# Performance work log

Measured on AMD Instinct MI355X. Metric: run time of the kernel, lower is better.

The kernel has to match this reference:

```python
import jax, jax.numpy as jnp
import numpy as np

N_CELLS = 50000
N_GENES = 2000
HIDDEN = 128
HEADS = 4
HEAD_DIM = HIDDEN // HEADS
E_FULL = 800000
E_PRUNED = 400000
LN_EPS = 1e-6
NEG_SLOPE = 0.2


def setup_inputs() -> dict:
    key = jax.random.key(0)
    ks = jax.random.split(key, 20)
    s_in = 1.0 / np.sqrt(N_GENES)
    s_h = 1.0 / np.sqrt(HIDDEN)
    inp = {
        "node_features": jax.random.normal(ks[0], (N_CELLS, N_GENES), jnp.float32),
        "full_edge_index": jax.random.randint(ks[1], (2, E_FULL), 0, N_CELLS, jnp.int64 if jax.config.jax_enable_x64 else jnp.int32),
        "full_edge_weights": jax.random.uniform(ks[2], (E_FULL, 1), jnp.float32),
        "pruned_edge_index": jax.random.randint(ks[3], (2, E_PRUNED), 0, N_CELLS, jnp.int64 if jax.config.jax_enable_x64 else jnp.int32),
        "pruned_edge_weights": jax.random.uniform(ks[4], (E_PRUNED, 1), jnp.float32),
        "alpha": jax.random.uniform(ks[5], (), jnp.float32),
        # input projection
        "ip_w": jax.random.normal(ks[6], (N_GENES, HIDDEN), jnp.float32) * s_in,
        "ip_b": jnp.zeros((HIDDEN,), jnp.float32),
        # GAT full graph
        "gf_wsrc": jax.random.normal(ks[7], (HIDDEN, HIDDEN), jnp.float32) * s_h,
        "gf_wdst": jax.random.normal(ks[8], (HIDDEN, HIDDEN), jnp.float32) * s_h,
        "gf_wedge": jax.random.normal(ks[9], (1, HIDDEN), jnp.float32),
        "gf_attn": jax.random.normal(ks[10], (HEADS, HEAD_DIM), jnp.float32) * (1.0 / np.sqrt(HEAD_DIM)),
        "gf_bias": jnp.zeros((HIDDEN,), jnp.float32),
        # GAT pruned graph
        "gp_wsrc": jax.random.normal(ks[11], (HIDDEN, HIDDEN), jnp.float32) * s_h,
        "gp_wdst": jax.random.normal(ks[12], (HIDDEN, HIDDEN), jnp.float32) * s_h,
        "gp_wedge": jax.random.normal(ks[13], (1, HIDDEN), jnp.float32),
        "gp_attn": jax.random.normal(ks[14], (HEADS, HEAD_DIM), jnp.float32) * (1.0 / np.sqrt(HEAD_DIM)),
        "gp_bias": jnp.zeros((HIDDEN,), jnp.float32),
        # LayerNorm
        "ln_scale": jnp.ones((HIDDEN,), jnp.float32),
        "ln_bias": jnp.zeros((HIDDEN,), jnp.float32),
    }
    return inp


def _gatv2(h, edge_index, edge_w, wsrc, wdst, wedge, attn, bias):
    """GATv2 with edge features: e_ij = a_h . leaky_relu(Ws h_i + Wd h_j + We w_ij),
    segment-softmax over destination nodes, scatter-aggregate Ws h_src, concat heads."""
    n = h.shape[0]
    src, dst = edge_index[0], edge_index[1]
    hs = (h @ wsrc).reshape(n, HEADS, HEAD_DIM)
    hd = (h @ wdst).reshape(n, HEADS, HEAD_DIM)
    ew = (edge_w @ wedge).reshape(-1, HEADS, HEAD_DIM)  # [E,H,D]
    z = jax.nn.leaky_relu(hs[src] + hd[dst] + ew, NEG_SLOPE)  # [E,H,D]
    logits = jnp.einsum('ehd,hd->eh', z, attn)  # [E,H]
    # segment softmax over incoming edges of each dst node
    m = jax.ops.segment_max(logits, dst, num_segments=n)
    m = jnp.where(jnp.isfinite(m), m, 0.0)
    ex = jnp.exp(logits - m[dst])
    denom = jax.ops.segment_sum(ex, dst, num_segments=n)
    att = ex / (denom[dst] + 1e-16)  # [E,H]
    out = jax.ops.segment_sum(att[..., None] * hs[src], dst, num_segments=n)  # [n,H,D]
    return out.reshape(n, HIDDEN) + bias


def _layer_norm(x, scale, bias):
    mu = jnp.mean(x, axis=-1, keepdims=True)
    var = jnp.mean(jnp.square(x - mu), axis=-1, keepdims=True)
    return (x - mu) * jax.lax.rsqrt(var + LN_EPS) * scale + bias


def reference(node_features, full_edge_index, full_edge_weights, pruned_edge_index,
              pruned_edge_weights, alpha, ip_w, ip_b,
              gf_wsrc, gf_wdst, gf_wedge, gf_attn, gf_bias,
              gp_wsrc, gp_wdst, gp_wedge, gp_attn, gp_bias,
              ln_scale, ln_bias):
    h = node_features @ ip_w + ip_b  # [n, hidden]
    h_full = _gatv2(h, full_edge_index, full_edge_weights, gf_wsrc, gf_wdst, gf_wedge, gf_attn, gf_bias)
    h_pruned = _gatv2(h, pruned_edge_index, pruned_edge_weights, gp_wsrc, gp_wdst, gp_wedge, gp_attn, gp_bias)
    h = (1.0 - alpha) * h_full + alpha * h_pruned
    h = jax.nn.elu(h)
    return _layer_norm(h, ln_scale, ln_bias)
```

## Files before the change

### kernel.cpp

```cpp
#include <hip/hip_runtime.h>

#define N_GENES 2000

typedef __attribute__((ext_vector_type(8))) short frag8;
typedef __attribute__((ext_vector_type(4))) float facc4;

static __device__ __forceinline__ unsigned short f2bf(float f) {
    unsigned int u = __float_as_uint(f);
    unsigned int r = (u + 0x7FFFu + ((u >> 16) & 1u)) >> 16;
    return (unsigned short)r;
}
static __device__ __forceinline__ float bf2f(unsigned short s) {
    return __uint_as_float(((unsigned int)s) << 16);
}

__global__ void transpose_bt(const float* __restrict__ W, unsigned short* __restrict__ Bt,
                             int K, int Kpad) {
    int idx = blockIdx.x * blockDim.x + threadIdx.x;
    if (idx >= 128 * Kpad) return;
    int nrow = idx / Kpad, k = idx - nrow * Kpad;
    unsigned short v = 0;
    if (k < K) v = f2bf(W[(size_t)k * 128 + nrow]);
    Bt[idx] = v;
}

__global__ void transpose_small(const float* __restrict__ ws_f, const float* __restrict__ wd_f,
                                const float* __restrict__ ws_p, const float* __restrict__ wd_p,
                                unsigned short* __restrict__ Bf, unsigned short* __restrict__ Bp) {
    int idx = blockIdx.x * blockDim.x + threadIdx.x;
    if (idx >= 2 * 256 * 128) return;
    int g = idx >> 15;
    int r = (idx >> 7) & 255;
    int k = idx & 127;
    const float* w = (g == 0) ? (r < 128 ? ws_f : wd_f) : (r < 128 ? ws_p : wd_p);
    unsigned short v = f2bf(w[k * 128 + (r & 127)]);
    (g == 0 ? Bf : Bp)[(r << 7) | k] = v;
}

#define SA 72

template <int AF32, int NT, int BIAS>
__global__ __launch_bounds__(256) void gemm64(const void* __restrict__ Av,
                                              const unsigned short* __restrict__ Bt,
                                              const float* __restrict__ bias,
                                              unsigned short* __restrict__ Cb,
                                              int M, int K, int Kpad) {
    __shared__ __align__(16) unsigned short lA[64 * SA];
    __shared__ __align__(16) unsigned short lB[NT * SA];
    constexpr int CF = NT / 64;
    int t = threadIdx.x, lane = t & 63, wv = t >> 6;
    int lr = lane & 15, lq = lane >> 4;
    facc4 acc[4][CF];
#pragma unroll
    for (int i = 0; i < 4; i++)
#pragma unroll
        for (int j = 0; j < CF; j++) acc[i][j] = (facc4){0.f, 0.f, 0.f, 0.f};
    int row_base = blockIdx.x * 64;

    for (int k0 = 0; k0 < Kpad; k0 += 64) {
        __syncthreads();
        if (AF32) {
            const float* A = (const float*)Av;
#pragma unroll
            for (int j = 0; j < 4; j++) {
                int q = j * 256 + t;
                int r = q >> 4, off = (q & 15) * 4;
                int rg = row_base + r; if (rg >= M) rg = M - 1;
                int kk = k0 + off;
                float4 v = {0.f, 0.f, 0.f, 0.f};
                if (kk < K) v = *(const float4*)(A + (size_t)rg * K + kk);
                ushort4 b;
                b.x = f2bf(v.x); b.y = f2bf(v.y); b.z = f2bf(v.z); b.w = f2bf(v.w);
                *(ushort4*)&lA[r * SA + off] = b;
            }
        } else {
            const unsigned short* A = (const unsigned short*)Av;
#pragma unroll
            for (int j = 0; j < 2; j++) {
                int q = j * 256 + t;
                int r = q >> 3, off = (q & 7) * 8;
                int rg = row_base + r; if (rg >= M) rg = M - 1;
                *(uint4*)&lA[r * SA + off] = *(const uint4*)(A + (size_t)rg * K + k0 + off);
            }
        }
#pragma unroll
        for (int j = 0; j < NT / 32; j++) {
            int q = j * 256 + t;
            int r = q >> 3, off = (q & 7) * 8;
            *(uint4*)&lB[r * SA + off] = *(const uint4*)(Bt + (size_t)r * Kpad + k0 + off);
        }
        __syncthreads();
#pragma unroll
        for (int ks = 0; ks < 2; ks++) {
            frag8 af[4], bf[CF];
#pragma unroll
            for (int mi = 0; mi < 4; mi++)
                af[mi] = *(const frag8*)&lA[(mi * 16 + lr) * SA + ks * 32 + lq * 8];
#pragma unroll
            for (int ni = 0; ni < CF; ni++)
                bf[ni] = *(const frag8*)&lB[(wv * 16 * CF + ni * 16 + lr) * SA + ks * 32 + lq * 8];
#pragma unroll
            for (int mi = 0; mi < 4; mi++)
#pragma unroll
                for (int ni = 0; ni < CF; ni++)
                    acc[mi][ni] = __builtin_amdgcn_mfma_f32_16x16x32_bf16(af[mi], bf[ni], acc[mi][ni], 0, 0, 0);
        }
    }
#pragma unroll
    for (int mi = 0; mi < 4; mi++) {
#pragma unroll
        for (int r = 0; r < 4; r++) {
            int row = row_base + mi * 16 + lq * 4 + r;
            if (row < M) {
#pragma unroll
                for (int ni = 0; ni < CF; ni++) {
                    int col = wv * 16 * CF + ni * 16 + lr;
                    float v = acc[mi][ni][r];
                    if (BIAS) v += bias[col];
                    Cb[(size_t)row * NT + col] = f2bf(v);
                }
            }
        }
    }
}

__global__ void deg2(const int* __restrict__ dst_f, int Ef,
                     const int* __restrict__ dst_p, int Ep,
                     int* __restrict__ deg, int N) {
    int e = blockIdx.x * blockDim.x + threadIdx.x;
    if (e < Ef) atomicAdd(&deg[dst_f[e]], 1);
    else if (e < Ef + Ep) atomicAdd(&deg[N + dst_p[e - Ef]], 1);
}

__global__ __launch_bounds__(256) void scan_part(const int* __restrict__ in,
                                                 int* __restrict__ bsum, int n) {
    int t = threadIdx.x, b = blockIdx.x;
    int lane = t & 63, wv = t >> 6;
    int base = b * 2048 + t * 8;
    int s = 0;
    if (base + 7 < n) {
        int4 v0 = *(const int4*)(in + base);
        int4 v1 = *(const int4*)(in + base + 4);
        s = v0.x + v0.y + v0.z + v0.w + v1.x + v1.y + v1.z + v1.w;
    } else {
#pragma unroll
        for (int j = 0; j < 8; j++) if (base + j < n) s += in[base + j];
    }
#pragma unroll
    for (int o = 32; o >= 1; o >>= 1) s += __shfl_xor(s, o);
    __shared__ int red[4];
    if (lane == 0) red[wv] = s;
    __syncthreads();
    if (t == 0) bsum[b] = red[0] + red[1] + red[2] + red[3];
}

__global__ __launch_bounds__(256) void scan_tops(int* __restrict__ bsum, int nb,
                                                 int* __restrict__ offs, int n) {
    __shared__ int buf[256];
    int t = threadIdx.x;
    int orig = (t < nb) ? bsum[t] : 0;
    int v = orig;
    buf[t] = v;
    __syncthreads();
    for (int o = 1; o < 256; o <<= 1) {
        int y = (t >= o) ? buf[t - o] : 0;
        __syncthreads();
        v += y;
        buf[t] = v;
        __syncthreads();
    }
    if (t < nb) bsum[t] = v - orig;
    if (t == nb - 1) offs[n] = v;
}

__global__ __launch_bounds__(256) void scan_final(const int* __restrict__ in,
                                                  const int* __restrict__ bsum,
                                                  int* __restrict__ offs, int n) {
    int t = threadIdx.x, b = blockIdx.x;
    int lane = t & 63, wv = t >> 6;
    int base = b * 2048 + t * 8;
    int a[8];
#pragma unroll
    for (int j = 0; j < 8; j++) a[j] = (base + j < n) ? in[base + j] : 0;
    int s = a[0] + a[1] + a[2] + a[3] + a[4] + a[5] + a[6] + a[7];
    int incl = s;
#pragma unroll
    for (int o = 1; o < 64; o <<= 1) {
        int y = __shfl_up(incl, o);
        if (lane >= o) incl += y;
    }
    __shared__ int wsum[4];
    if (lane == 63) wsum[wv] = incl;
    __syncthreads();
    int wpre = 0;
#pragma unroll
    for (int j = 0; j < 4; j++) if (j < wv) wpre += wsum[j];
    int excl = incl - s + wpre + bsum[b];
#pragma unroll
    for (int j = 0; j < 8; j++) {
        if (base + j < n) offs[base + j] = excl;
        excl += a[j];
    }
}

__global__ void fill2(const int* __restrict__ src_f, const int* __restrict__ dst_f,
                      const float* __restrict__ ew_f, int Ef,
                      const int* __restrict__ src_p, const int* __restrict__ dst_p,
                      const float* __restrict__ ew_p, int Ep,
                      const int* __restrict__ offs, int* __restrict__ cur,
                      int* __restrict__ srcs, float* __restrict__ ws, int N) {
    int e = blockIdx.x * blockDim.x + threadIdx.x;
    if (e >= Ef + Ep) return;
    int g = (e >= Ef);
    int ee = g ? e - Ef : e;
    int d = g ? dst_p[ee] : dst_f[ee];
    int node = g ? N + d : d;
    int p = offs[node] + atomicAdd(&cur[node], 1);
    srcs[p] = g ? src_p[ee] : src_f[ee];
    ws[p] = g ? ew_p[ee] : ew_f[ee];
}

__global__ __launch_bounds__(256) void gat_kernel(const int* __restrict__ offs,
                                                  const int* __restrict__ srcs,
                                                  const float* __restrict__ ws,
                                                  const unsigned short* __restrict__ hshd,
                                                  const float* __restrict__ wedge,
                                                  const float* __restrict__ attn,
                                                  const float* __restrict__ bias,
                                                  float* __restrict__ out, int n) {
    int node = blockIdx.x * 4 + (threadIdx.x >> 6);
    if (node >= n) return;
    int lane = threadIdx.x & 63;
    const float wv0 = wedge[lane], wv1 = wedge[lane + 64];
    const float a0 = attn[lane], a1 = attn[lane + 64];
    const unsigned short* hdrow = hshd + (size_t)node * 256 + 128;
    const float hd0 = bf2f(hdrow[lane]);
    const float hd1 = bf2f(hdrow[lane + 64]);
    int s = offs[node], cnt = offs[node + 1] - s;
    float m0 = -INFINITY, l0 = 0.f, acc0 = 0.f;
    float m1 = -INFINITY, l1 = 0.f, acc1 = 0.f;
    if (cnt > 0) {
        int last = s + cnt - 1;
        int jB = (s + 1 <= last) ? s + 1 : last;
        int srcA = srcs[s];       float wA = ws[s];
        int srcB = srcs[jB];      float wB = ws[jB];
        float hsA0 = bf2f(hshd[(size_t)srcA * 256 + lane]);
        float hsA1 = bf2f(hshd[(size_t)srcA * 256 + 64 + lane]);
        float hsB0 = bf2f(hshd[(size_t)srcB * 256 + lane]);
        float hsB1 = bf2f(hshd[(size_t)srcB * 256 + 64 + lane]);
        for (int i = 0; i < cnt; i++) {
            int jC = s + i + 2; if (jC > last) jC = last;
            int srcC = srcs[jC];  float wC = ws[jC];
            float hsC0 = bf2f(hshd[(size_t)srcC * 256 + lane]);
            float hsC1 = bf2f(hshd[(size_t)srcC * 256 + 64 + lane]);
            float z0 = hsA0 + hd0 + wA * wv0; z0 = (z0 > 0.f) ? z0 : 0.2f * z0;
            float z1 = hsA1 + hd1 + wA * wv1; z1 = (z1 > 0.f) ? z1 : 0.2f * z1;
            float t0 = z0 * a0, t1 = z1 * a1;
#pragma unroll
            for (int o = 16; o >= 1; o >>= 1) {
                t0 += __shfl_xor(t0, o);
                t1 += __shfl_xor(t1, o);
            }
            float mn0 = fmaxf(m0, t0), mn1 = fmaxf(m1, t1);
            float sc0 = __expf(m0 - mn0), sc1 = __expf(m1 - mn1);
            float p0 = __expf(t0 - mn0), p1 = __expf(t1 - mn1);
            l0 = l0 * sc0 + p0; acc0 = acc0 * sc0 + p0 * hsA0; m0 = mn0;
            l1 = l1 * sc1 + p1; acc1 = acc1 * sc1 + p1 * hsA1; m1 = mn1;
            hsA0 = hsB0; hsA1 = hsB1; wA = wB;
            hsB0 = hsC0; hsB1 = hsC1; wB = wC;
        }
    }
    out[(size_t)node * 128 + lane] = acc0 / (l0 + 1e-16f) + bias[lane];
    out[(size_t)node * 128 + 64 + lane] = acc1 / (l1 + 1e-16f) + bias[lane + 64];
}

__global__ __launch_bounds__(256) void final_kernel(const float* __restrict__ hf,
                                                    float* __restrict__ out,
                                                    const float* __restrict__ alpha_p,
                                                    const float* __restrict__ scale,
                                                    const float* __restrict__ beta, int n) {
    int node = blockIdx.x * 4 + (threadIdx.x >> 6);
    if (node >= n) return;
    int lane = threadIdx.x & 63;
    float a = *alpha_p;
    float f0 = hf[(size_t)node * 128 + lane], f1 = hf[(size_t)node * 128 + 64 + lane];
    float p0 = out[(size_t)node * 128 + lane], p1 = out[(size_t)node * 128 + 64 + lane];
    float x0 = (1.f - a) * f0 + a * p0;
    float x1 = (1.f - a) * f1 + a * p1;
    x0 = (x0 > 0.f) ? x0 : expm1f(x0);
    x1 = (x1 > 0.f) ? x1 : expm1f(x1);
    float sm = x0 + x1;
#pragma unroll
    for (int o = 32; o >= 1; o >>= 1) sm += __shfl_xor(sm, o);
    float mu = sm * (1.f / 128.f);
    float d0 = x0 - mu, d1 = x1 - mu;
    float v = d0 * d0 + d1 * d1;
#pragma unroll
    for (int o = 32; o >= 1; o >>= 1) v += __shfl_xor(v, o);
    float rstd = rsqrtf(v * (1.f / 128.f) + 1e-6f);
    out[(size_t)node * 128 + lane] = d0 * rstd * scale[lane] + beta[lane];
    out[(size_t)node * 128 + 64 + lane] = d1 * rstd * scale[lane + 64] + beta[lane + 64];
}

extern "C" void kernel_launch(void* const* d_in, const int* in_sizes, int n_in,
                              void* d_out, int out_size, void* d_ws, size_t ws_size,
                              hipStream_t stream) {
    const float* nf = (const float*)d_in[0];
    const int* fei = (const int*)d_in[1];
    const float* few = (const float*)d_in[2];
    const int* pei = (const int*)d_in[3];
    const float* pew = (const float*)d_in[4];
    const float* alpha = (const float*)d_in[5];
    const float* ip_w = (const float*)d_in[6];
    const float* ip_b = (const float*)d_in[7];
    const float* gf_wsrc = (const float*)d_in[8];
    const float* gf_wdst = (const float*)d_in[9];
    const float* gf_wedge = (const float*)d_in[10];
    const float* gf_attn = (const float*)d_in[11];
    const float* gf_bias = (const float*)d_in[12];
    const float* gp_wsrc = (const float*)d_in[13];
    const float* gp_wdst = (const float*)d_in[14];
    const float* gp_wedge = (const float*)d_in[15];
    const float* gp_attn = (const float*)d_in[16];
    const float* gp_bias = (const float*)d_in[17];
    const float* ln_scale = (const float*)d_in[18];
    const float* ln_bias = (const float*)d_in[19];

    const int N = in_sizes[0] / N_GENES;
    const int Ef = in_sizes[1] / 2;
    const int Ep = in_sizes[3] / 2;
    const int Etot = Ef + Ep;
    const int Kpad1 = 2048;
    const int n2 = 2 * N;

    char* base = (char*)d_ws;
    size_t off = 0;
    auto carve = [&](size_t bytes) -> char* {
        char* p = base + off;
        off = (off + bytes + 255) & ~(size_t)255;
        return p;
    };
    unsigned short* Bt1 = (unsigned short*)carve((size_t)128 * Kpad1 * 2);
    unsigned short* Bf = (unsigned short*)carve(256 * 128 * 2);
    unsigned short* Bp = (unsigned short*)carve(256 * 128 * 2);
    unsigned short* h_bf = (unsigned short*)carve((size_t)N * 128 * 2);
    unsigned short* hshd_f = (unsigned short*)carve((size_t)N * 256 * 2);
    unsigned short* hshd_p = (unsigned short*)carve((size_t)N * 256 * 2);
    float* h_full = (float*)carve((size_t)N * 128 * 4);
    int* deg = (int*)carve((size_t)n2 * 4);
    int* offs = (int*)carve((size_t)(n2 + 4) * 4);
    int* cur = (int*)carve((size_t)n2 * 4);
    int* bsum = (int*)carve(256 * 4);
    int* srcs = (int*)carve((size_t)Etot * 4);
    float* wso = (float*)carve((size_t)Etot * 4);
    float* out_f = (float*)d_out;

    transpose_bt<<<(128 * Kpad1 + 255) / 256, 256, 0, stream>>>(ip_w, Bt1, N_GENES, Kpad1);
    transpose_small<<<(2 * 256 * 128 + 255) / 256, 256, 0, stream>>>(gf_wsrc, gf_wdst, gp_wsrc, gp_wdst, Bf, Bp);

    int gb1 = (N + 63) / 64;
    gemm64<1, 128, 1><<<gb1, 256, 0, stream>>>(nf, Bt1, ip_b, h_bf, N, N_GENES, Kpad1);
    gemm64<0, 256, 0><<<gb1, 256, 0, stream>>>(h_bf, Bf, nullptr, hshd_f, N, 128, 128);
    gemm64<0, 256, 0><<<gb1, 256, 0, stream>>>(h_bf, Bp, nullptr, hshd_p, N, 128, 128);

    const int* src_f = fei;
    const int* dst_f = fei + Ef;
    const int* src_p = pei;
    const int* dst_p = pei + Ep;
    hipMemsetAsync(deg, 0, (size_t)n2 * 4, stream);
    deg2<<<(Etot + 255) / 256, 256, 0, stream>>>(dst_f, Ef, dst_p, Ep, deg, N);
    int nb = (n2 + 2047) / 2048;
    scan_part<<<nb, 256, 0, stream>>>(deg, bsum, n2);
    scan_tops<<<1, 256, 0, stream>>>(bsum, nb, offs, n2);
    scan_final<<<nb, 256, 0, stream>>>(deg, bsum, offs, n2);
    hipMemsetAsync(cur, 0, (size_t)n2 * 4, stream);
    fill2<<<(Etot + 255) / 256, 256, 0, stream>>>(src_f, dst_f, few, Ef, src_p, dst_p, pew, Ep,
                                                  offs, cur, srcs, wso, N);

    int nodeblocks = (N + 3) / 4;
    gat_kernel<<<nodeblocks, 256, 0, stream>>>(offs, srcs, wso, hshd_f,
                                               gf_wedge, gf_attn, gf_bias, h_full, N);
    gat_kernel<<<nodeblocks, 256, 0, stream>>>(offs + N, srcs, wso, hshd_p,
                                               gp_wedge, gp_attn, gp_bias, out_f, N);

    final_kernel<<<nodeblocks, 256, 0, stream>>>(h_full, out_f, alpha, ln_scale, ln_bias, N);
    (void)ws_size; (void)n_in; (void)out_size;
}
```

Before: 972.9 us.

## Merge kernels, prefetch GEMM operands, pack CSR edges, and unroll GAT aggregation

The two weight transposes become one prep kernel, and the two small projection GEMMs become a single launch using a 2-D grid. The input-projection GEMM now register-prefetches the next K tile of A and holds B fragments in registers rather than staging them through LDS. The CSR fill reuses the degree counters with decrementing atomics, which drops the cursor memset, and it packs source and weight into one int2 array. Both GAT passes run in a single launch with deeper gather prefetch and two edges processed per iteration. The cost is higher register pressure and B fragments loaded straight from global memory, which adds global traffic per block.

```diff
diff --git a/kernel.cpp b/kernel.cpp
--- a/kernel.cpp
+++ b/kernel.cpp
@@ -1,6 +1,8 @@
 #include <hip/hip_runtime.h>
+#include <hip/hip_bf16.h>
 
 #define N_GENES 2000
+#define SA 72
 
 typedef __attribute__((ext_vector_type(8))) short frag8;
 typedef __attribute__((ext_vector_type(4))) float facc4;
@@ -13,41 +15,141 @@
 static __device__ __forceinline__ float bf2f(unsigned short s) {
     return __uint_as_float(((unsigned int)s) << 16);
 }
-
-__global__ void transpose_bt(const float* __restrict__ W, unsigned short* __restrict__ Bt,
-                             int K, int Kpad) {
+static __device__ __forceinline__ ushort2 pk2(float a, float b) {
+    __hip_bfloat162 r = __float22bfloat162_rn(float2{a, b});
+    return *(ushort2*)&r;
+}
+
+__global__ void prep(const float* __restrict__ ip_w,
+                     const float* __restrict__ ws_f, const float* __restrict__ wd_f,
+                     const float* __restrict__ ws_p, const float* __restrict__ wd_p,
+                     unsigned short* __restrict__ Bt1,
+                     unsigned short* __restrict__ Bf, unsigned short* __restrict__ Bp) {
     int idx = blockIdx.x * blockDim.x + threadIdx.x;
-    if (idx >= 128 * Kpad) return;
-    int nrow = idx / Kpad, k = idx - nrow * Kpad;
-    unsigned short v = 0;
-    if (k < K) v = f2bf(W[(size_t)k * 128 + nrow]);
-    Bt[idx] = v;
-}
-
-__global__ void transpose_small(const float* __restrict__ ws_f, const float* __restrict__ wd_f,
-                                const float* __restrict__ ws_p, const float* __restrict__ wd_p,
-                                unsigned short* __restrict__ Bf, unsigned short* __restrict__ Bp) {
-    int idx = blockIdx.x * blockDim.x + threadIdx.x;
-    if (idx >= 2 * 256 * 128) return;
-    int g = idx >> 15;
-    int r = (idx >> 7) & 255;
-    int k = idx & 127;
-    const float* w = (g == 0) ? (r < 128 ? ws_f : wd_f) : (r < 128 ? ws_p : wd_p);
-    unsigned short v = f2bf(w[k * 128 + (r & 127)]);
-    (g == 0 ? Bf : Bp)[(r << 7) | k] = v;
-}
-
-#define SA 72
-
-template <int AF32, int NT, int BIAS>
-__global__ __launch_bounds__(256) void gemm64(const void* __restrict__ Av,
-                                              const unsigned short* __restrict__ Bt,
-                                              const float* __restrict__ bias,
-                                              unsigned short* __restrict__ Cb,
-                                              int M, int K, int Kpad) {
+    if (idx < 128 * 2048) {
+        int nrow = idx >> 11, k = idx & 2047;
+        unsigned short v = 0;
+        if (k < N_GENES) v = f2bf(ip_w[(size_t)k * 128 + nrow]);
+        Bt1[idx] = v;
+    } else {
+        int q = idx - 128 * 2048;
+        if (q >= 2 * 256 * 128) return;
+        int g = q >> 15;
+        int r = (q >> 7) & 255;
+        int k = q & 127;
+        const float* w = (g == 0) ? (r < 128 ? ws_f : wd_f) : (r < 128 ? ws_p : wd_p);
+        (g == 0 ? Bf : Bp)[(r << 7) | k] = f2bf(w[k * 128 + (r & 127)]);
+    }
+}
+
+__global__ __launch_bounds__(256) void gemm1(const float* __restrict__ A,
+                                             const unsigned short* __restrict__ Bt,
+                                             const float* __restrict__ bias,
+                                             unsigned short* __restrict__ Cb, int M, int K) {
+    const int Kpad = 2048;
+    __shared__ __align__(16) unsigned short lA[64 * SA];
+    int t = threadIdx.x, lane = t & 63, wv = t >> 6;
+    int lr = lane & 15, lq = lane >> 4;
+    facc4 acc[4][2];
+#pragma unroll
+    for (int i = 0; i < 4; i++)
+#pragma unroll
+        for (int j = 0; j < 2; j++) acc[i][j] = (facc4){0.f, 0.f, 0.f, 0.f};
+    int row_base = blockIdx.x * 64;
+
+    int ar_r[4], ar_c[4];
+    const float* ar_p[4];
+#pragma unroll
+    for (int j = 0; j < 4; j++) {
+        int q = j * 256 + t;
+        ar_r[j] = q >> 4;
+        ar_c[j] = (q & 15) * 4;
+        int rg = row_base + ar_r[j];
+        if (rg >= M) rg = M - 1;
+        ar_p[j] = A + (size_t)rg * K + ar_c[j];
+    }
+    const unsigned short* bp[4];
+#pragma unroll
+    for (int ks = 0; ks < 2; ks++)
+#pragma unroll
+        for (int ni = 0; ni < 2; ni++) {
+            int col = wv * 32 + ni * 16 + lr;
+            bp[ks * 2 + ni] = Bt + (size_t)col * Kpad + ks * 32 + lq * 8;
+        }
+
+    float4 ar[4];
+    frag8 bfr[4];
+#pragma unroll
+    for (int j = 0; j < 4; j++) ar[j] = *(const float4*)(ar_p[j]);
+#pragma unroll
+    for (int f = 0; f < 4; f++) bfr[f] = *(const frag8*)(bp[f]);
+
+    for (int k0 = 0; k0 < Kpad; k0 += 64) {
+        __syncthreads();
+#pragma unroll
+        for (int j = 0; j < 4; j++) {
+            ushort2 u01 = pk2(ar[j].x, ar[j].y);
+            ushort2 u23 = pk2(ar[j].z, ar[j].w);
+            ushort4 u = {u01.x, u01.y, u23.x, u23.y};
+            *(ushort4*)&lA[ar_r[j] * SA + ar_c[j]] = u;
+        }
+        __syncthreads();
+        int kn = k0 + 64;
+        frag8 bfn[4];
+        if (kn < Kpad) {
+#pragma unroll
+            for (int j = 0; j < 4; j++) {
+                int kk = kn + ar_c[j];
+                float4 v = {0.f, 0.f, 0.f, 0.f};
+                if (kk < K) v = *(const float4*)(ar_p[j] + kn);
+                ar[j] = v;
+            }
+#pragma unroll
+            for (int f = 0; f < 4; f++) bfn[f] = *(const frag8*)(bp[f] + kn);
+        }
+#pragma unroll
+        for (int ks = 0; ks < 2; ks++) {
+            frag8 af[4];
+#pragma unroll
+            for (int mi = 0; mi < 4; mi++)
+                af[mi] = *(const frag8*)&lA[(mi * 16 + lr) * SA + ks * 32 + lq * 8];
+#pragma unroll
+            for (int mi = 0; mi < 4; mi++)
+#pragma unroll
+                for (int ni = 0; ni < 2; ni++)
+                    acc[mi][ni] = __builtin_amdgcn_mfma_f32_16x16x32_bf16(af[mi], bfr[ks * 2 + ni], acc[mi][ni], 0, 0, 0);
+        }
+        if (kn < Kpad) {
+#pragma unroll
+            for (int f = 0; f < 4; f++) bfr[f] = bfn[f];
+        }
+    }
+#pragma unroll
+    for (int mi = 0; mi < 4; mi++) {
+#pragma unroll
+        for (int r = 0; r < 4; r++) {
+            int row = row_base + mi * 16 + lq * 4 + r;
+            if (row < M) {
+#pragma unroll
+                for (int ni = 0; ni < 2; ni++) {
+                    int col = wv * 32 + ni * 16 + lr;
+                    Cb[(size_t)row * 128 + col] = f2bf(acc[mi][ni][r] + bias[col]);
+                }
+            }
+        }
+    }
+}
+
+__global__ __launch_bounds__(256) void gemm_hshd(const unsigned short* __restrict__ A,
+                                                 const unsigned short* __restrict__ Bf,
+                                                 const unsigned short* __restrict__ Bp,
+                                                 unsigned short* __restrict__ Cf,
+                                                 unsigned short* __restrict__ Cp, int M) {
+    const int K = 128, NT = 256, CF = 4;
+    const unsigned short* Bt = blockIdx.y ? Bp : Bf;
+    unsigned short* Cb = blockIdx.y ? Cp : Cf;
     __shared__ __align__(16) unsigned short lA[64 * SA];
     __shared__ __align__(16) unsigned short lB[NT * SA];
-    constexpr int CF = NT / 64;
     int t = threadIdx.x, lane = t & 63, wv = t >> 6;
     int lr = lane & 15, lq = lane >> 4;
     facc4 acc[4][CF];
@@ -57,37 +159,20 @@
         for (int j = 0; j < CF; j++) acc[i][j] = (facc4){0.f, 0.f, 0.f, 0.f};
     int row_base = blockIdx.x * 64;
 
-    for (int k0 = 0; k0 < Kpad; k0 += 64) {
-        __syncthreads();
-        if (AF32) {
-            const float* A = (const float*)Av;
-#pragma unroll
-            for (int j = 0; j < 4; j++) {
-                int q = j * 256 + t;
-                int r = q >> 4, off = (q & 15) * 4;
-                int rg = row_base + r; if (rg >= M) rg = M - 1;
-                int kk = k0 + off;
-                float4 v = {0.f, 0.f, 0.f, 0.f};
-                if (kk < K) v = *(const float4*)(A + (size_t)rg * K + kk);
-                ushort4 b;
-                b.x = f2bf(v.x); b.y = f2bf(v.y); b.z = f2bf(v.z); b.w = f2bf(v.w);
-                *(ushort4*)&lA[r * SA + off] = b;
-            }
-        } else {
-            const unsigned short* A = (const unsigned short*)Av;
-#pragma unroll
-            for (int j = 0; j < 2; j++) {
-                int q = j * 256 + t;
-                int r = q >> 3, off = (q & 7) * 8;
-                int rg = row_base + r; if (rg >= M) rg = M - 1;
-                *(uint4*)&lA[r * SA + off] = *(const uint4*)(A + (size_t)rg * K + k0 + off);
-            }
-        }
-#pragma unroll
-        for (int j = 0; j < NT / 32; j++) {
+    for (int k0 = 0; k0 < K; k0 += 64) {
+        __syncthreads();
+#pragma unroll
+        for (int j = 0; j < 2; j++) {
             int q = j * 256 + t;
             int r = q >> 3, off = (q & 7) * 8;
-            *(uint4*)&lB[r * SA + off] = *(const uint4*)(Bt + (size_t)r * Kpad + k0 + off);
+            int rg = row_base + r; if (rg >= M) rg = M - 1;
+            *(uint4*)&lA[r * SA + off] = *(const uint4*)(A + (size_t)rg * K + k0 + off);
+        }
+#pragma unroll
+        for (int j = 0; j < 8; j++) {
+            int q = j * 256 + t;
+            int r = q >> 3, off = (q & 7) * 8;
+            *(uint4*)&lB[r * SA + off] = *(const uint4*)(Bt + (size_t)r * K + k0 + off);
         }
         __syncthreads();
 #pragma unroll
@@ -115,9 +200,7 @@
 #pragma unroll
                 for (int ni = 0; ni < CF; ni++) {
                     int col = wv * 16 * CF + ni * 16 + lr;
-                    float v = acc[mi][ni][r];
-                    if (BIAS) v += bias[col];
-                    Cb[(size_t)row * NT + col] = f2bf(v);
+                    Cb[(size_t)row * NT + col] = f2bf(acc[mi][ni][r]);
                 }
             }
         }
@@ -207,71 +290,103 @@
                       const float* __restrict__ ew_f, int Ef,
                       const int* __restrict__ src_p, const int* __restrict__ dst_p,
                       const float* __restrict__ ew_p, int Ep,
-                      const int* __restrict__ offs, int* __restrict__ cur,
-                      int* __restrict__ srcs, float* __restrict__ ws, int N) {
+                      const int* __restrict__ offs, int* __restrict__ deg,
+                      int2* __restrict__ srcw, int N) {
     int e = blockIdx.x * blockDim.x + threadIdx.x;
     if (e >= Ef + Ep) return;
     int g = (e >= Ef);
     int ee = g ? e - Ef : e;
     int d = g ? dst_p[ee] : dst_f[ee];
     int node = g ? N + d : d;
-    int p = offs[node] + atomicAdd(&cur[node], 1);
-    srcs[p] = g ? src_p[ee] : src_f[ee];
-    ws[p] = g ? ew_p[ee] : ew_f[ee];
-}
-
-__global__ __launch_bounds__(256) void gat_kernel(const int* __restrict__ offs,
-                                                  const int* __restrict__ srcs,
-                                                  const float* __restrict__ ws,
-                                                  const unsigned short* __restrict__ hshd,
-                                                  const float* __restrict__ wedge,
-                                                  const float* __restrict__ attn,
-                                                  const float* __restrict__ bias,
-                                                  float* __restrict__ out, int n) {
+    int p = offs[node] + atomicAdd(&deg[node], -1) - 1;
+    int s = g ? src_p[ee] : src_f[ee];
+    float w = g ? ew_p[ee] : ew_f[ee];
+    srcw[p] = make_int2(s, __float_as_int(w));
+}
+
+__global__ __launch_bounds__(256) void gat2(const int* __restrict__ offs,
+                                            const int2* __restrict__ srcw,
+                                            const unsigned short* __restrict__ hshd_f,
+                                            const unsigned short* __restrict__ hshd_p,
+                                            const float* __restrict__ wedge_f,
+                                            const float* __restrict__ attn_f,
+                                            const float* __restrict__ bias_f,
+                                            const float* __restrict__ wedge_p,
+                                            const float* __restrict__ attn_p,
+                                            const float* __restrict__ bias_p,
+                                            float* __restrict__ out_full,
+                                            float* __restrict__ out_pruned, int N) {
     int node = blockIdx.x * 4 + (threadIdx.x >> 6);
-    if (node >= n) return;
+    if (node >= 2 * N) return;
+    int g = node >= N;
+    int onode = g ? node - N : node;
+    const unsigned short* hshd = g ? hshd_p : hshd_f;
+    const float* wedge = g ? wedge_p : wedge_f;
+    const float* attn = g ? attn_p : attn_f;
+    const float* bias = g ? bias_p : bias_f;
+    float* out = g ? out_pruned : out_full;
     int lane = threadIdx.x & 63;
     const float wv0 = wedge[lane], wv1 = wedge[lane + 64];
     const float a0 = attn[lane], a1 = attn[lane + 64];
-    const unsigned short* hdrow = hshd + (size_t)node * 256 + 128;
-    const float hd0 = bf2f(hdrow[lane]);
-    const float hd1 = bf2f(hdrow[lane + 64]);
+    const float hd0 = bf2f(hshd[(size_t)onode * 256 + 128 + lane]);
+    const float hd1 = bf2f(hshd[(size_t)onode * 256 + 192 + lane]);
     int s = offs[node], cnt = offs[node + 1] - s;
     float m0 = -INFINITY, l0 = 0.f, acc0 = 0.f;
     float m1 = -INFINITY, l1 = 0.f, acc1 = 0.f;
     if (cnt > 0) {
         int last = s + cnt - 1;
-        int jB = (s + 1 <= last) ? s + 1 : last;
-        int srcA = srcs[s];       float wA = ws[s];
-        int srcB = srcs[jB];      float wB = ws[jB];
-        float hsA0 = bf2f(hshd[(size_t)srcA * 256 + lane]);
-        float hsA1 = bf2f(hshd[(size_t)srcA * 256 + 64 + lane]);
-        float hsB0 = bf2f(hshd[(size_t)srcB * 256 + lane]);
-        float hsB1 = bf2f(hshd[(size_t)srcB * 256 + 64 + lane]);
-        for (int i = 0; i < cnt; i++) {
-            int jC = s + i + 2; if (jC > last) jC = last;
-            int srcC = srcs[jC];  float wC = ws[jC];
-            float hsC0 = bf2f(hshd[(size_t)srcC * 256 + lane]);
-            float hsC1 = bf2f(hshd[(size_t)srcC * 256 + 64 + lane]);
-            float z0 = hsA0 + hd0 + wA * wv0; z0 = (z0 > 0.f) ? z0 : 0.2f * z0;
-            float z1 = hsA1 + hd1 + wA * wv1; z1 = (z1 > 0.f) ? z1 : 0.2f * z1;
-            float t0 = z0 * a0, t1 = z1 * a1;
+        auto CL = [last](int j) { return j > last ? last : j; };
+        int2 e0 = srcw[s], e1 = srcw[CL(s + 1)], e2 = srcw[CL(s + 2)], e3 = srcw[CL(s + 3)];
+        float h00 = bf2f(hshd[(size_t)e0.x * 256 + lane]);
+        float h01 = bf2f(hshd[(size_t)e0.x * 256 + 64 + lane]);
+        float h10 = bf2f(hshd[(size_t)e1.x * 256 + lane]);
+        float h11 = bf2f(hshd[(size_t)e1.x * 256 + 64 + lane]);
+        float h20 = bf2f(hshd[(size_t)e2.x * 256 + lane]);
+        float h21 = bf2f(hshd[(size_t)e2.x * 256 + 64 + lane]);
+        float h30 = bf2f(hshd[(size_t)e3.x * 256 + lane]);
+        float h31 = bf2f(hshd[(size_t)e3.x * 256 + 64 + lane]);
+        for (int i = 0; i < cnt; i += 2) {
+            int2 e4 = srcw[CL(s + i + 4)], e5 = srcw[CL(s + i + 5)];
+            float h40 = bf2f(hshd[(size_t)e4.x * 256 + lane]);
+            float h41 = bf2f(hshd[(size_t)e4.x * 256 + 64 + lane]);
+            float h50 = bf2f(hshd[(size_t)e5.x * 256 + lane]);
+            float h51 = bf2f(hshd[(size_t)e5.x * 256 + 64 + lane]);
+            float w0 = __int_as_float(e0.y), w1 = __int_as_float(e1.y);
+            float z00 = h00 + hd0 + w0 * wv0; z00 = (z00 > 0.f) ? z00 : 0.2f * z00;
+            float z01 = h01 + hd1 + w0 * wv1; z01 = (z01 > 0.f) ? z01 : 0.2f * z01;
+            float z10 = h10 + hd0 + w1 * wv0; z10 = (z10 > 0.f) ? z10 : 0.2f * z10;
+            float z11 = h11 + hd1 + w1 * wv1; z11 = (z11 > 0.f) ? z11 : 0.2f * z11;
+            float t00 = z00 * a0, t01 = z01 * a1;
+            float t10 = z10 * a0, t11 = z11 * a1;
 #pragma unroll
             for (int o = 16; o >= 1; o >>= 1) {
-                t0 += __shfl_xor(t0, o);
-                t1 += __shfl_xor(t1, o);
-            }
-            float mn0 = fmaxf(m0, t0), mn1 = fmaxf(m1, t1);
-            float sc0 = __expf(m0 - mn0), sc1 = __expf(m1 - mn1);
-            float p0 = __expf(t0 - mn0), p1 = __expf(t1 - mn1);
-            l0 = l0 * sc0 + p0; acc0 = acc0 * sc0 + p0 * hsA0; m0 = mn0;
-            l1 = l1 * sc1 + p1; acc1 = acc1 * sc1 + p1 * hsA1; m1 = mn1;
-            hsA0 = hsB0; hsA1 = hsB1; wA = wB;
-            hsB0 = hsC0; hsB1 = hsC1; wB = wC;
-        }
-    }
-    out[(size_t)node * 128 + lane] = acc0 / (l0 + 1e-16f) + bias[lane];
-    out[(size_t)node * 128 + 64 + lane] = acc1 / (l1 + 1e-16f) + bias[lane + 64];
+                t00 += __shfl_xor(t00, o);
+                t01 += __shfl_xor(t01, o);
+                t10 += __shfl_xor(t10, o);
+                t11 += __shfl_xor(t11, o);
+            }
+            {
+                float mn0 = fmaxf(m0, t00), mn1 = fmaxf(m1, t01);
+                float sc0 = __expf(m0 - mn0), sc1 = __expf(m1 - mn1);
+                float p0 = __expf(t00 - mn0), p1 = __expf(t01 - mn1);
+                l0 = l0 * sc0 + p0; acc0 = acc0 * sc0 + p0 * h00; m0 = mn0;
+                l1 = l1 * sc1 + p1; acc1 = acc1 * sc1 + p1 * h01; m1 = mn1;
+            }
+            if (i + 1 < cnt) {
+                float mn0 = fmaxf(m0, t10), mn1 = fmaxf(m1, t11);
+                float sc0 = __expf(m0 - mn0), sc1 = __expf(m1 - mn1);
+                float p0 = __expf(t10 - mn0), p1 = __expf(t11 - mn1);
+                l0 = l0 * sc0 + p0; acc0 = acc0 * sc0 + p0 * h10; m0 = mn0;
+                l1 = l1 * sc1 + p1; acc1 = acc1 * sc1 + p1 * h11; m1 = mn1;
+            }
+            e0 = e2; h00 = h20; h01 = h21;
+            e1 = e3; h10 = h30; h11 = h31;
+            e2 = e4; h20 = h40; h21 = h41;
+            e3 = e5; h30 = h50; h31 = h51;
+        }
+    }
+    out[(size_t)onode * 128 + lane] = acc0 / (l0 + 1e-16f) + bias[lane];
+    out[(size_t)onode * 128 + 64 + lane] = acc1 / (l1 + 1e-16f) + bias[lane + 64];
 }
 
 __global__ __launch_bounds__(256) void final_kernel(const float* __restrict__ hf,
@@ -330,7 +445,6 @@
     const int Ef = in_sizes[1] / 2;
     const int Ep = in_sizes[3] / 2;
     const int Etot = Ef + Ep;
-    const int Kpad1 = 2048;
     const int n2 = 2 * N;
 
     char* base = (char*)d_ws;
@@ -340,7 +454,7 @@
         off = (off + bytes + 255) & ~(size_t)255;
         return p;
     };
-    unsigned short* Bt1 = (unsigned short*)carve((size_t)128 * Kpad1 * 2);
+    unsigned short* Bt1 = (unsigned short*)carve((size_t)128 * 2048 * 2);
     unsigned short* Bf = (unsigned short*)carve(256 * 128 * 2);
     unsigned short* Bp = (unsigned short*)carve(256 * 128 * 2);
     unsigned short* h_bf = (unsigned short*)carve((size_t)N * 128 * 2);
@@ -349,19 +463,16 @@
     float* h_full = (float*)carve((size_t)N * 128 * 4);
     int* deg = (int*)carve((size_t)n2 * 4);
     int* offs = (int*)carve((size_t)(n2 + 4) * 4);
-    int* cur = (int*)carve((size_t)n2 * 4);
     int* bsum = (int*)carve(256 * 4);
-    int* srcs = (int*)carve((size_t)Etot * 4);
-    float* wso = (float*)carve((size_t)Etot * 4);
+    int2* srcw = (int2*)carve((size_t)Etot * 8);
     float* out_f = (float*)d_out;
 
-    transpose_bt<<<(128 * Kpad1 + 255) / 256, 256, 0, stream>>>(ip_w, Bt1, N_GENES, Kpad1);
-    transpose_small<<<(2 * 256 * 128 + 255) / 256, 256, 0, stream>>>(gf_wsrc, gf_wdst, gp_wsrc, gp_wdst, Bf, Bp);
+    prep<<<(128 * 2048 + 2 * 256 * 128 + 255) / 256, 256, 0, stream>>>(
+        ip_w, gf_wsrc, gf_wdst, gp_wsrc, gp_wdst, Bt1, Bf, Bp);
 
     int gb1 = (N + 63) / 64;
-    gemm64<1, 128, 1><<<gb1, 256, 0, stream>>>(nf, Bt1, ip_b, h_bf, N, N_GENES, Kpad1);
-    gemm64<0, 256, 0><<<gb1, 256, 0, stream>>>(h_bf, Bf, nullptr, hshd_f, N, 128, 128);
-    gemm64<0, 256, 0><<<gb1, 256, 0, stream>>>(h_bf, Bp, nullptr, hshd_p, N, 128, 128);
+    gemm1<<<gb1, 256, 0, stream>>>(nf, Bt1, ip_b, h_bf, N, N_GENES);
+    gemm_hshd<<<dim3(gb1, 2), 256, 0, stream>>>(h_bf, Bf, Bp, hshd_f, hshd_p, N);
 
     const int* src_f = fei;
     const int* dst_f = fei + Ef;
@@ -373,16 +484,14 @@
     scan_part<<<nb, 256, 0, stream>>>(deg, bsum, n2);
     scan_tops<<<1, 256, 0, stream>>>(bsum, nb, offs, n2);
     scan_final<<<nb, 256, 0, stream>>>(deg, bsum, offs, n2);
-    hipMemsetAsync(cur, 0, (size_t)n2 * 4, stream);
     fill2<<<(Etot + 255) / 256, 256, 0, stream>>>(src_f, dst_f, few, Ef, src_p, dst_p, pew, Ep,
-                                                  offs, cur, srcs, wso, N);
-
-    int nodeblocks = (N + 3) / 4;
-    gat_kernel<<<nodeblocks, 256, 0, stream>>>(offs, srcs, wso, hshd_f,
-                                               gf_wedge, gf_attn, gf_bias, h_full, N);
-    gat_kernel<<<nodeblocks, 256, 0, stream>>>(offs + N, srcs, wso, hshd_p,
-                                               gp_wedge, gp_attn, gp_bias, out_f, N);
-
-    final_kernel<<<nodeblocks, 256, 0, stream>>>(h_full, out_f, alpha, ln_scale, ln_bias, N);
+                                                  offs, deg, srcw, N);
+
+    gat2<<<(n2 + 3) / 4, 256, 0, stream>>>(offs, srcw, hshd_f, hshd_p,
+                                           gf_wedge, gf_attn, gf_bias,
+                                           gp_wedge, gp_attn, gp_bias,
+                                           h_full, out_f, N);
+
+    final_kernel<<<(N + 3) / 4, 256, 0, stream>>>(h_full, out_f, alpha, ln_scale, ln_bias, N);
     (void)ws_size; (void)n_in; (void)out_size;
 }
```

Measured after the change: 915.6 us. 5.9% less time.
